# Kernel tuning notes

Measured on AMD Instinct MI355X. Metric: run time of the kernel, lower is better.

## Reference

```python
import jax, jax.numpy as jnp
import numpy as np

B, S, H = 16, 4096, 768
NUM_WORDS = S // 2  # 2048: max distinct words per sample (padded output width)


def setup_inputs() -> dict:
    key = jax.random.key(0)
    k1, k2 = jax.random.split(key)
    hidden_states = jax.random.normal(k1, (B, S, H), dtype=jnp.float32)
    # word ids: non-decreasing, contiguous from 0; -1 marks special tokens (None in HF)
    inc = jax.random.bernoulli(k2, 0.5, (B, S)).astype(jnp.int32)
    inc = inc.at[:, :2].set(0)  # keep word 0 alive at position 1 after masking CLS
    word_ids = jnp.maximum(jnp.cumsum(inc, axis=1) - 1, 0)
    word_ids = jnp.minimum(word_ids, NUM_WORDS - 1)  # static cap on segment count
    word_ids = word_ids.at[:, 0].set(-1)   # [CLS]
    word_ids = word_ids.at[:, -1].set(-1)  # [SEP]
    return {"hidden_states": hidden_states, "word_ids": word_ids}


def reference(hidden_states, word_ids):
    # Segment-mean of subword embeddings into word embeddings.
    # hidden_states: [B, S, H] float; word_ids: [B, S] int, -1 = special token (dropped).
    b, s, h = hidden_states.shape
    valid = word_ids >= 0  # [B, S]
    # offset per-sample word ids into a flat segment space of size B*NUM_WORDS;
    # invalid tokens go to segment (b*NUM_WORDS + 0) but contribute zeros.
    wid = jnp.where(valid, word_ids, 0)
    seg = (wid + jnp.arange(b, dtype=word_ids.dtype)[:, None] * NUM_WORDS).reshape(-1)
    data = jnp.where(valid[..., None], hidden_states, 0.0).reshape(b * s, h)
    sums = jax.ops.segment_sum(data, seg, num_segments=b * NUM_WORDS)
    counts = jax.ops.segment_sum(
        valid.reshape(-1).astype(hidden_states.dtype), seg, num_segments=b * NUM_WORDS
    )
    sums = sums.reshape(b, NUM_WORDS, h)
    counts = counts.reshape(b, NUM_WORDS)
    # mean per word; words with zero tokens stay 0 (matches pad_sequence zero-padding)
    return sums / jnp.maximum(counts, 1.0)[..., None]
```

## Files before the change

kernel.cpp:

```cpp
#include <hip/hip_runtime.h>

constexpr int B = 16;
constexpr int S = 4096;
constexpr int H = 768;
constexpr int NW = 2048;
constexpr int VEC_PER_ROW = H / 4;

__global__ __launch_bounds__(256)
void find_starts_kernel(const int* __restrict__ wid, int* __restrict__ starts) {
    const int idx = blockIdx.x * 256 + threadIdx.x;
    const int s = idx & (S - 1);
    const int b = idx >> 12;
    if (s < 1 || s >= S - 1) return;
    const int* __restrict__ row = wid + (size_t)b * S;
    const int cur = row[s];
    const int prev = row[s - 1];
    if (cur != prev && cur >= 0) {
        starts[b * NW + cur] = s;
    }
}

__global__ __launch_bounds__(VEC_PER_ROW)
void seg_mean_kernel(const float* __restrict__ hs,
                     const int* __restrict__ wid,
                     const int* __restrict__ starts,
                     float* __restrict__ out) {
    const int blk = blockIdx.x;
    const int b = blk >> 11;
    const int w = blk & (NW - 1);
    const int t = threadIdx.x;

    float4* __restrict__ o = (float4*)(out + (size_t)blk * H);

    const int maxw = wid[(size_t)b * S + (S - 2)];

    if (w > maxw) {
        o[t] = make_float4(0.f, 0.f, 0.f, 0.f);
        return;
    }

    const int start = starts[blk];
    const int end = (w == maxw) ? (S - 1) : starts[blk + 1];
    const int cnt = end - start;

    const float4* __restrict__ base = (const float4*)(hs + (size_t)b * S * H);

    float4 acc = make_float4(0.f, 0.f, 0.f, 0.f);
    for (int s = start; s < end; ++s) {
        float4 v = base[(size_t)s * VEC_PER_ROW + t];
        acc.x += v.x; acc.y += v.y; acc.z += v.z; acc.w += v.w;
    }

    const float inv = 1.0f / (float)cnt;
    acc.x *= inv; acc.y *= inv; acc.z *= inv; acc.w *= inv;
    o[t] = acc;
}

extern "C" void kernel_launch(void* const* d_in, const int* in_sizes, int n_in,
                              void* d_out, int out_size, void* d_ws, size_t ws_size,
                              hipStream_t stream) {
    const float* hs = (const float*)d_in[0];
    const int* wid = (const int*)d_in[1];
    float* out = (float*)d_out;
    int* starts = (int*)d_ws;

    find_starts_kernel<<<(B * S) / 256, 256, 0, stream>>>(wid, starts);
    seg_mean_kernel<<<B * NW, VEC_PER_ROW, 0, stream>>>(hs, wid, starts, out);
}
```

Before: 342.5 us.

## Map one wave per word segment and unroll token accumulation by two

The segment-mean kernel now assigns one 64-lane wave to each word, with each lane handling three float4 chunks of the row, and packs 16 words into a 1024-thread block instead of one 192-thread block per word. The accumulation loop processes two tokens per iteration, so six independent loads are in flight per lane. The aim is to cut block launch overhead and raise memory-level parallelism in a bandwidth-bound reduction. Register use per thread rises and blocks are coarser, which may reduce scheduling flexibility.

```diff
diff --git a/kernel.cpp b/kernel.cpp
--- a/kernel.cpp
+++ b/kernel.cpp
@@ -4,7 +4,8 @@
 constexpr int S = 4096;
 constexpr int H = 768;
 constexpr int NW = 2048;
-constexpr int VEC_PER_ROW = H / 4;
+constexpr int V4 = H / 4;
+constexpr int WAVES_PER_BLK = 16;
 
 __global__ __launch_bounds__(256)
 void find_starts_kernel(const int* __restrict__ wid, int* __restrict__ starts) {
@@ -14,28 +15,27 @@
     if (s < 1 || s >= S - 1) return;
     const int* __restrict__ row = wid + (size_t)b * S;
     const int cur = row[s];
-    const int prev = row[s - 1];
-    if (cur != prev && cur >= 0) {
-        starts[b * NW + cur] = s;
-    }
+    if (cur != row[s - 1] && cur >= 0) starts[b * NW + cur] = s;
 }
 
-__global__ __launch_bounds__(VEC_PER_ROW)
+__global__ __launch_bounds__(64 * WAVES_PER_BLK)
 void seg_mean_kernel(const float* __restrict__ hs,
                      const int* __restrict__ wid,
                      const int* __restrict__ starts,
                      float* __restrict__ out) {
-    const int blk = blockIdx.x;
+    const int wave = threadIdx.x >> 6;
+    const int lane = threadIdx.x & 63;
+    const int blk = blockIdx.x * WAVES_PER_BLK + wave;
     const int b = blk >> 11;
     const int w = blk & (NW - 1);
-    const int t = threadIdx.x;
 
     float4* __restrict__ o = (float4*)(out + (size_t)blk * H);
 
     const int maxw = wid[(size_t)b * S + (S - 2)];
 
     if (w > maxw) {
-        o[t] = make_float4(0.f, 0.f, 0.f, 0.f);
+        float4 z = make_float4(0.f, 0.f, 0.f, 0.f);
+        o[lane] = z; o[lane + 64] = z; o[lane + 128] = z;
         return;
     }
 
@@ -45,15 +45,35 @@
 
     const float4* __restrict__ base = (const float4*)(hs + (size_t)b * S * H);
 
-    float4 acc = make_float4(0.f, 0.f, 0.f, 0.f);
-    for (int s = start; s < end; ++s) {
-        float4 v = base[(size_t)s * VEC_PER_ROW + t];
-        acc.x += v.x; acc.y += v.y; acc.z += v.z; acc.w += v.w;
+    float4 a0 = make_float4(0.f, 0.f, 0.f, 0.f);
+    float4 a1 = a0, a2 = a0;
+
+    int s = start;
+    for (; s + 1 < end; s += 2) {
+        const float4* p0 = base + (size_t)s * V4;
+        const float4* p1 = p0 + V4;
+        float4 v0 = p0[lane], v1 = p0[lane + 64], v2 = p0[lane + 128];
+        float4 u0 = p1[lane], u1 = p1[lane + 64], u2 = p1[lane + 128];
+        a0.x += v0.x; a0.y += v0.y; a0.z += v0.z; a0.w += v0.w;
+        a1.x += v1.x; a1.y += v1.y; a1.z += v1.z; a1.w += v1.w;
+        a2.x += v2.x; a2.y += v2.y; a2.z += v2.z; a2.w += v2.w;
+        a0.x += u0.x; a0.y += u0.y; a0.z += u0.z; a0.w += u0.w;
+        a1.x += u1.x; a1.y += u1.y; a1.z += u1.z; a1.w += u1.w;
+        a2.x += u2.x; a2.y += u2.y; a2.z += u2.z; a2.w += u2.w;
+    }
+    if (s < end) {
+        const float4* p0 = base + (size_t)s * V4;
+        float4 v0 = p0[lane], v1 = p0[lane + 64], v2 = p0[lane + 128];
+        a0.x += v0.x; a0.y += v0.y; a0.z += v0.z; a0.w += v0.w;
+        a1.x += v1.x; a1.y += v1.y; a1.z += v1.z; a1.w += v1.w;
+        a2.x += v2.x; a2.y += v2.y; a2.z += v2.z; a2.w += v2.w;
     }
 
     const float inv = 1.0f / (float)cnt;
-    acc.x *= inv; acc.y *= inv; acc.z *= inv; acc.w *= inv;
-    o[t] = acc;
+    a0.x *= inv; a0.y *= inv; a0.z *= inv; a0.w *= inv;
+    a1.x *= inv; a1.y *= inv; a1.z *= inv; a1.w *= inv;
+    a2.x *= inv; a2.y *= inv; a2.z *= inv; a2.w *= inv;
+    o[lane] = a0; o[lane + 64] = a1; o[lane + 128] = a2;
 }
 
 extern "C" void kernel_launch(void* const* d_in, const int* in_sizes, int n_in,
@@ -65,5 +85,6 @@
     int* starts = (int*)d_ws;
 
     find_starts_kernel<<<(B * S) / 256, 256, 0, stream>>>(wid, starts);
-    seg_mean_kernel<<<B * NW, VEC_PER_ROW, 0, stream>>>(hs, wid, starts, out);
+    seg_mean_kernel<<<(B * NW) / WAVES_PER_BLK, 64 * WAVES_PER_BLK, 0, stream>>>(
+        hs, wid, starts, out);
 }
```

After: 330.9 us. -3.4%, faster.
